# Kernel tuning notes

Measured on AMD Instinct MI355X. Metric: run time of the kernel, lower is better.

Reference implementation:

```python
import jax, jax.numpy as jnp
import numpy as np

HIDDEN = 1024
FFN = 4096
NUM_EXPERTS = 8
TOP_K = 2


def setup_inputs() -> dict:
    key = jax.random.key(0)
    k1, k2, k3, k4, k5 = jax.random.split(key, 5)
    B, T = 4, 2048
    x = jax.random.normal(k1, (B, T, HIDDEN), dtype=jnp.float32)
    # router: nn.Linear(hidden_dim, num_experts)
    bound = 1.0 / np.sqrt(HIDDEN)
    router_w = jax.random.uniform(k2, (NUM_EXPERTS, HIDDEN), dtype=jnp.float32, minval=-bound, maxval=bound)
    router_b = jax.random.uniform(k3, (NUM_EXPERTS,), dtype=jnp.float32, minval=-bound, maxval=bound)
    w1 = jax.random.normal(k4, (NUM_EXPERTS, HIDDEN, FFN), dtype=jnp.float32) * 0.02
    w2 = jax.random.normal(k5, (NUM_EXPERTS, FFN, HIDDEN), dtype=jnp.float32) * 0.02
    return {"x": x, "router_w": router_w, "router_b": router_b, "w1": w1, "w2": w2}


def reference(x, router_w, router_b, w1, w2):
    B, T, H = x.shape
    x_flat = x.reshape(-1, H)                      # [N, H], N = B*T
    logits = x_flat @ router_w.T + router_b        # [N, E]
    probs = jax.nn.softmax(logits, axis=-1)
    topk_w, topk_idx = jax.lax.top_k(probs, TOP_K)  # [N, K]
    topk_w = topk_w / jnp.sum(topk_w, axis=-1, keepdims=True)
    # combine weight per (expert, token): sum_k topk_w[:,k] * onehot(topk_idx[:,k])
    onehot = jax.nn.one_hot(topk_idx, NUM_EXPERTS, dtype=x.dtype)   # [N, K, E]
    combine = jnp.einsum('nk,nke->en', topk_w, onehot)              # [E, N]
    # dense per-expert FFN (math identical to original masked loop: gelu(0)=0)
    hidden = jax.nn.gelu(jnp.einsum('nh,ehf->enf', x_flat, w1), approximate=False)  # [E, N, F]
    expert_out = jnp.einsum('enf,efh->enh', hidden, w2)             # [E, N, H]
    out = jnp.einsum('enh,en->nh', expert_out, combine)             # [N, H]
    return out.reshape(B, T, H)
```

## Files before the change

### kernel.cpp

```cpp
#include <hip/hip_runtime.h>
#include <cstdint>
#include <cstddef>

#define H_DIM 1024
#define F_DIM 4096
#define N_EXP 8
#define N_TOK 8192
#define NK_ASSIGN (N_TOK * 2)
#define MAX_MB 24
#define NMB 32

typedef unsigned short u16;
typedef __attribute__((ext_vector_type(8))) short bf16x8;
typedef __attribute__((ext_vector_type(4))) float f32x4;

__device__ __forceinline__ u16 f2bf(float f) {
  unsigned int u = __float_as_uint(f);
  u += 0x7fffu + ((u >> 16) & 1u);
  return (u16)(u >> 16);
}

__device__ __forceinline__ void load16(const u16* g, u16* l) {
  __builtin_amdgcn_global_load_lds(
      (const __attribute__((address_space(1))) void*)g,
      (__attribute__((address_space(3))) void*)l, 16, 0, 0);
}

__global__ __launch_bounds__(256) void router_kernel(
    const float* __restrict__ x, const float* __restrict__ rw,
    const float* __restrict__ rb, int* __restrict__ topk_idx,
    float* __restrict__ topk_w, u16* __restrict__ xb) {
  const int lane = threadIdx.x & 63;
  const int wid = threadIdx.x >> 6;
  const int t = blockIdx.x * 4 + wid;
  const float4* xr = (const float4*)(x + (size_t)t * H_DIM);
  u16* xo = xb + (size_t)t * H_DIM;
  float acc[N_EXP];
#pragma unroll
  for (int e = 0; e < N_EXP; ++e) acc[e] = 0.f;
#pragma unroll
  for (int j = 0; j < 4; ++j) {
    float4 xv = xr[j * 64 + lane];
    ushort4 u;
    u.x = f2bf(xv.x); u.y = f2bf(xv.y); u.z = f2bf(xv.z); u.w = f2bf(xv.w);
    *(ushort4*)(xo + (size_t)(j * 64 + lane) * 4) = u;
#pragma unroll
    for (int e = 0; e < N_EXP; ++e) {
      float4 wv = ((const float4*)(rw + e * H_DIM))[j * 64 + lane];
      acc[e] += xv.x * wv.x + xv.y * wv.y + xv.z * wv.z + xv.w * wv.w;
    }
  }
#pragma unroll
  for (int off = 32; off > 0; off >>= 1) {
#pragma unroll
    for (int e = 0; e < N_EXP; ++e) acc[e] += __shfl_xor(acc[e], off);
  }
  if (lane == 0) {
    float lg[N_EXP];
#pragma unroll
    for (int e = 0; e < N_EXP; ++e) lg[e] = acc[e] + rb[e];
    int i0 = 0;
    float b0 = lg[0];
#pragma unroll
    for (int e = 1; e < N_EXP; ++e)
      if (lg[e] > b0) { b0 = lg[e]; i0 = e; }
    int i1 = -1;
    float b1 = -3.4e38f;
#pragma unroll
    for (int e = 0; e < N_EXP; ++e)
      if (e != i0 && lg[e] > b1) { b1 = lg[e]; i1 = e; }
    float w0 = 1.f / (1.f + __expf(b1 - b0));
    topk_idx[2 * t] = i0;
    topk_idx[2 * t + 1] = i1;
    topk_w[2 * t] = w0;
    topk_w[2 * t + 1] = 1.f - w0;
  }
}

__global__ __launch_bounds__(256) void hist_kernel(
    const int* __restrict__ topk_idx, int* __restrict__ hist_g) {
  __shared__ int hh[N_EXP];
  const int tid = threadIdx.x;
  if (tid < N_EXP) hh[tid] = 0;
  __syncthreads();
  const int t = blockIdx.x * 256 + tid;
  const int e0 = topk_idx[2 * t], e1 = topk_idx[2 * t + 1];
  atomicAdd(&hh[e0], 1);
  atomicAdd(&hh[e1], 1);
  __syncthreads();
  if (tid < N_EXP) hist_g[blockIdx.x * N_EXP + tid] = hh[tid];
}

__global__ __launch_bounds__(256) void scan_kernel(
    const int* __restrict__ hist_g, int* __restrict__ offsets,
    int* __restrict__ pos_base) {
  __shared__ int sh[NMB * N_EXP];
  __shared__ int pb[NMB * N_EXP];
  const int tid = threadIdx.x;
  sh[tid] = hist_g[tid];
  __syncthreads();
  if (tid == 0) {
    int tot[N_EXP];
    for (int e = 0; e < N_EXP; ++e) tot[e] = 0;
    for (int b = 0; b < NMB; ++b)
      for (int e = 0; e < N_EXP; ++e) tot[e] += sh[b * N_EXP + e];
    int run = 0;
    for (int e = 0; e < N_EXP; ++e) { offsets[e] = run; run += tot[e]; }
    offsets[N_EXP] = run;
    for (int e = 0; e < N_EXP; ++e) {
      int r = offsets[e];
      for (int b = 0; b < NMB; ++b) { pb[b * N_EXP + e] = r; r += sh[b * N_EXP + e]; }
    }
  }
  __syncthreads();
  pos_base[tid] = pb[tid];
}

__global__ __launch_bounds__(256) void scatter_kernel(
    const int* __restrict__ topk_idx, const float* __restrict__ topk_w,
    const int* __restrict__ pos_base, int* __restrict__ assign_token,
    float* __restrict__ assign_gate, int* __restrict__ slot_of) {
  __shared__ int cur[N_EXP];
  __shared__ int pb[N_EXP];
  const int tid = threadIdx.x;
  if (tid < N_EXP) {
    cur[tid] = 0;
    pb[tid] = pos_base[blockIdx.x * N_EXP + tid];
  }
  __syncthreads();
  const int t = blockIdx.x * 256 + tid;
#pragma unroll
  for (int k = 0; k < 2; ++k) {
    int e = topk_idx[2 * t + k];
    int local = atomicAdd(&cur[e], 1);
    int pos = pb[e] + local;
    assign_token[pos] = t;
    assign_gate[pos] = topk_w[2 * t + k];
    slot_of[2 * t + k] = pos;
  }
}

__global__ __launch_bounds__(256) void transpose_cvt(
    const float* __restrict__ in, u16* __restrict__ out, int R, int C) {
  __shared__ u16 lds[64 * 66];
  const int e = blockIdx.z;
  const float* ip = in + (size_t)e * R * C;
  u16* op = out + (size_t)e * R * C;
  const int c0 = blockIdx.x * 64, r0 = blockIdx.y * 64;
  const int tid = threadIdx.x;
  const int tx = tid & 15, ty = tid >> 4;
#pragma unroll
  for (int i = 0; i < 4; ++i) {
    const int r = ty + i * 16;
    float4 v = *(const float4*)(ip + (size_t)(r0 + r) * C + c0 + tx * 4);
    ushort2 u01, u23;
    u01.x = f2bf(v.x); u01.y = f2bf(v.y);
    u23.x = f2bf(v.z); u23.y = f2bf(v.w);
    *(ushort2*)&lds[r * 66 + tx * 4] = u01;
    *(ushort2*)&lds[r * 66 + tx * 4 + 2] = u23;
  }
  __syncthreads();
  const int lane = tid & 63, wid = tid >> 6;
  const int r8 = lane & 7;
#pragma unroll
  for (int s = 0; s < 2; ++s) {
    const int c = s * 32 + wid * 8 + (lane >> 3);
    union { u16 u[8]; uint4 q; } pk;
#pragma unroll
    for (int k = 0; k < 8; ++k) pk.u[k] = lds[(r8 * 8 + k) * 66 + c];
    *(uint4*)(op + (size_t)(c0 + c) * R + r0 + r8 * 8) = pk.q;
  }
}

template <int LDA, int LDB, int LDC, int KITERS, int NXB, bool FIRST>
__global__ __launch_bounds__(256) void moe_gemm(
    const u16* __restrict__ Abase, const u16* __restrict__ Bbase,
    u16* __restrict__ hout, float* __restrict__ yout,
    const int* __restrict__ offsets, const float* __restrict__ assign_gate,
    const int* __restrict__ atok) {
  __shared__ __align__(16) u16 As[128 * 32];
  __shared__ __align__(16) u16 Bs[128 * 32];
  const int flat = blockIdx.x + NXB * (blockIdx.y + MAX_MB * blockIdx.z);
  const int e = flat & 7;
  const int s = flat >> 3;
  const int mb = s % MAX_MB;
  const int n0b = s / MAX_MB;
  const int row0 = offsets[e];
  const int cnt = offsets[e + 1] - row0;
  const int mbase = mb * 128;
  if (mbase >= cnt) return;
  const int mrem = cnt - mbase;
  const int n0 = n0b * 128;
  const int tid = threadIdx.x;
  const int lane = tid & 63;
  const int wid = tid >> 6;
  const int wm = wid & 1, wn = wid >> 1;
  const u16* B = Bbase + (size_t)e * ((size_t)H_DIM * F_DIM);
  const int row16 = lane & 15, quad = lane >> 4;
  const int srow = lane >> 2;
  const int scol = (lane & 3) * 8;

  const u16* Arow[2];
  const u16* Brow[2];
#pragma unroll
  for (int i = 0; i < 2; ++i) {
    const int c = wid * 2 + i;
    const int r = c * 16 + srow;
    const int ra = min(r, mrem - 1);
    if (FIRST) {
      const int tok = atok[row0 + mbase + ra];
      Arow[i] = Abase + (size_t)tok * LDA;
    } else {
      Arow[i] = Abase + (size_t)(row0 + mbase + ra) * LDA;
    }
    Brow[i] = B + (size_t)(n0 + r) * LDB;
  }

  f32x4 acc[4][4];
#pragma unroll
  for (int i = 0; i < 4; ++i)
#pragma unroll
    for (int j = 0; j < 4; ++j)
#pragma unroll
      for (int r = 0; r < 4; ++r) acc[i][j][r] = 0.f;

  for (int kt = 0; kt < KITERS; ++kt) {
    const int k0 = kt * 32;
#pragma unroll
    for (int i = 0; i < 2; ++i) {
      const int c = wid * 2 + i;
      load16(Arow[i] + k0 + scol, &As[c * 512]);
      load16(Brow[i] + k0 + scol, &Bs[c * 512]);
    }
    __syncthreads();
    bf16x8 av[4], bv[4];
#pragma unroll
    for (int mi = 0; mi < 4; ++mi)
      av[mi] = *(const bf16x8*)&As[(wm * 64 + mi * 16 + row16) * 32 + quad * 8];
#pragma unroll
    for (int ni = 0; ni < 4; ++ni)
      bv[ni] = *(const bf16x8*)&Bs[(wn * 64 + ni * 16 + row16) * 32 + quad * 8];
#pragma unroll
    for (int mi = 0; mi < 4; ++mi)
#pragma unroll
      for (int ni = 0; ni < 4; ++ni)
        acc[mi][ni] =
            __builtin_amdgcn_mfma_f32_16x16x32_bf16(av[mi], bv[ni], acc[mi][ni], 0, 0, 0);
    __syncthreads();
  }

  if (FIRST) {
    u16* Cp = hout + (size_t)(row0 + mbase) * LDC + n0;
#pragma unroll
    for (int mi = 0; mi < 4; ++mi) {
#pragma unroll
      for (int r = 0; r < 4; ++r) {
        const int lm = wm * 64 + mi * 16 + quad * 4 + r;
        if (lm < mrem) {
#pragma unroll
          for (int ni = 0; ni < 4; ++ni) {
            float v = acc[mi][ni][r];
            float t = v * (0.7978845608028654f + 0.0356774081363f * v * v);
            v = v / (1.f + __expf(-2.f * t));
            Cp[(size_t)lm * LDC + (wn * 64 + ni * 16 + row16)] = f2bf(v);
          }
        }
      }
    }
  } else {
#pragma unroll
    for (int mi = 0; mi < 4; ++mi) {
#pragma unroll
      for (int r = 0; r < 4; ++r) {
        const int lm = wm * 64 + mi * 16 + quad * 4 + r;
        if (lm < mrem) {
          const int slot = row0 + mbase + lm;
          const float g = assign_gate[slot];
          float* orow = yout + (size_t)slot * LDC + n0;
#pragma unroll
          for (int ni = 0; ni < 4; ++ni)
            orow[wn * 64 + ni * 16 + row16] = acc[mi][ni][r] * g;
        }
      }
    }
  }
}

__global__ __launch_bounds__(256) void combine_kernel(
    const float* __restrict__ ys, const int* __restrict__ slot_of,
    float* __restrict__ out) {
  const int t = blockIdx.x;
  const int s0 = slot_of[2 * t], s1 = slot_of[2 * t + 1];
  const int i = threadIdx.x;
  float4 a = ((const float4*)(ys + (size_t)s0 * H_DIM))[i];
  float4 b = ((const float4*)(ys + (size_t)s1 * H_DIM))[i];
  float4 o;
  o.x = a.x + b.x; o.y = a.y + b.y; o.z = a.z + b.z; o.w = a.w + b.w;
  ((float4*)(out + (size_t)t * H_DIM))[i] = o;
}

extern "C" void kernel_launch(void* const* d_in, const int* in_sizes, int n_in,
                              void* d_out, int out_size, void* d_ws, size_t ws_size,
                              hipStream_t stream) {
  const float* x = (const float*)d_in[0];
  const float* rw = (const float*)d_in[1];
  const float* rb = (const float*)d_in[2];
  const float* w1 = (const float*)d_in[3];
  const float* w2 = (const float*)d_in[4];
  float* out = (float*)d_out;

  char* ws = (char*)d_ws;
  u16* w1b = (u16*)(ws);
  float* y_slot = (float*)(ws);
  u16* w2b = (u16*)(ws + 67108864);
  u16* xb = (u16*)(ws + 134217728);
  u16* h = (u16*)(ws + 167772160);
  int* hist_g = (int*)(ws + 167772160);
  int* pos_base = hist_g + NMB * N_EXP;
  char* meta = ws + 301989888;
  int* offsets = (int*)(meta + 64);
  int* topk_idx = (int*)(meta + 128);
  float* topk_w = (float*)(meta + 128 + 65536);
  int* assign_token = (int*)(meta + 128 + 131072);
  float* assign_gate = (float*)(meta + 128 + 196608);
  int* slot_of = (int*)(meta + 128 + 262144);

  router_kernel<<<N_TOK / 4, 256, 0, stream>>>(x, rw, rb, topk_idx, topk_w, xb);
  hist_kernel<<<NMB, 256, 0, stream>>>(topk_idx, hist_g);
  scan_kernel<<<1, 256, 0, stream>>>(hist_g, offsets, pos_base);
  scatter_kernel<<<NMB, 256, 0, stream>>>(topk_idx, topk_w, pos_base,
                                          assign_token, assign_gate, slot_of);
  transpose_cvt<<<dim3(F_DIM / 64, H_DIM / 64, N_EXP), 256, 0, stream>>>(w1, w1b, H_DIM, F_DIM);
  transpose_cvt<<<dim3(H_DIM / 64, F_DIM / 64, N_EXP), 256, 0, stream>>>(w2, w2b, F_DIM, H_DIM);

  moe_gemm<H_DIM, H_DIM, F_DIM, H_DIM / 32, F_DIM / 128, true>
      <<<dim3(F_DIM / 128, MAX_MB, N_EXP), 256, 0, stream>>>(
          xb, w1b, h, nullptr, offsets, assign_gate, assign_token);
  moe_gemm<F_DIM, F_DIM, H_DIM, F_DIM / 32, H_DIM / 128, false>
      <<<dim3(H_DIM / 128, MAX_MB, N_EXP), 256, 0, stream>>>(
          h, w2b, nullptr, y_slot, offsets, assign_gate, nullptr);
  combine_kernel<<<N_TOK, 256, 0, stream>>>(y_slot, slot_of, out);

  (void)in_sizes; (void)n_in; (void)ws_size;
}
```

Measured before the change: 803.3 us.

## Double GEMM K-tile to 64 with XOR-swizzled LDS and fuse scan into scatter

The MoE GEMM now stages a 64-wide K slice per iteration instead of 32, halving the number of barrier pairs per tile, and uses an XOR swizzle on the LDS column chunks to avoid bank conflicts on the 128-byte rows. Separately, the single-block scan kernel is removed: each scatter block recomputes the prefix totals from the histogram itself, saving one launch. The trade-off is double the LDS footprint per block and redundant scan work in every scatter block.

```diff
diff --git a/kernel.cpp b/kernel.cpp
--- a/kernel.cpp
+++ b/kernel.cpp
@@ -91,13 +91,17 @@
   if (tid < N_EXP) hist_g[blockIdx.x * N_EXP + tid] = hh[tid];
 }
 
-__global__ __launch_bounds__(256) void scan_kernel(
+__global__ __launch_bounds__(256) void scatter_kernel(
+    const int* __restrict__ topk_idx, const float* __restrict__ topk_w,
     const int* __restrict__ hist_g, int* __restrict__ offsets,
-    int* __restrict__ pos_base) {
+    int* __restrict__ assign_token, float* __restrict__ assign_gate,
+    int* __restrict__ slot_of) {
   __shared__ int sh[NMB * N_EXP];
-  __shared__ int pb[NMB * N_EXP];
+  __shared__ int pb[N_EXP];
+  __shared__ int cur[N_EXP];
   const int tid = threadIdx.x;
   sh[tid] = hist_g[tid];
+  if (tid < N_EXP) cur[tid] = 0;
   __syncthreads();
   if (tid == 0) {
     int tot[N_EXP];
@@ -105,27 +109,14 @@
     for (int b = 0; b < NMB; ++b)
       for (int e = 0; e < N_EXP; ++e) tot[e] += sh[b * N_EXP + e];
     int run = 0;
-    for (int e = 0; e < N_EXP; ++e) { offsets[e] = run; run += tot[e]; }
-    offsets[N_EXP] = run;
     for (int e = 0; e < N_EXP; ++e) {
-      int r = offsets[e];
-      for (int b = 0; b < NMB; ++b) { pb[b * N_EXP + e] = r; r += sh[b * N_EXP + e]; }
-    }
-  }
-  __syncthreads();
-  pos_base[tid] = pb[tid];
-}
-
-__global__ __launch_bounds__(256) void scatter_kernel(
-    const int* __restrict__ topk_idx, const float* __restrict__ topk_w,
-    const int* __restrict__ pos_base, int* __restrict__ assign_token,
-    float* __restrict__ assign_gate, int* __restrict__ slot_of) {
-  __shared__ int cur[N_EXP];
-  __shared__ int pb[N_EXP];
-  const int tid = threadIdx.x;
-  if (tid < N_EXP) {
-    cur[tid] = 0;
-    pb[tid] = pos_base[blockIdx.x * N_EXP + tid];
+      if (blockIdx.x == 0) offsets[e] = run;
+      int r = run;
+      for (int b = 0; b < (int)blockIdx.x; ++b) r += sh[b * N_EXP + e];
+      pb[e] = r;
+      run += tot[e];
+    }
+    if (blockIdx.x == 0) offsets[N_EXP] = run;
   }
   __syncthreads();
   const int t = blockIdx.x * 256 + tid;
@@ -178,8 +169,8 @@
     u16* __restrict__ hout, float* __restrict__ yout,
     const int* __restrict__ offsets, const float* __restrict__ assign_gate,
     const int* __restrict__ atok) {
-  __shared__ __align__(16) u16 As[128 * 32];
-  __shared__ __align__(16) u16 Bs[128 * 32];
+  __shared__ __align__(16) u16 As[128 * 64];
+  __shared__ __align__(16) u16 Bs[128 * 64];
   const int flat = blockIdx.x + NXB * (blockIdx.y + MAX_MB * blockIdx.z);
   const int e = flat & 7;
   const int s = flat >> 3;
@@ -197,23 +188,23 @@
   const int wm = wid & 1, wn = wid >> 1;
   const u16* B = Bbase + (size_t)e * ((size_t)H_DIM * F_DIM);
   const int row16 = lane & 15, quad = lane >> 4;
-  const int srow = lane >> 2;
-  const int scol = (lane & 3) * 8;
-
-  const u16* Arow[2];
-  const u16* Brow[2];
-#pragma unroll
-  for (int i = 0; i < 2; ++i) {
-    const int c = wid * 2 + i;
-    const int r = c * 16 + srow;
+  const int sr = lane >> 3;
+  const int scol = ((lane & 7) ^ sr) * 8;
+
+  const u16* Arow[4];
+  const u16* Brow[4];
+#pragma unroll
+  for (int i = 0; i < 4; ++i) {
+    const int c = wid * 4 + i;
+    const int r = c * 8 + sr;
     const int ra = min(r, mrem - 1);
     if (FIRST) {
       const int tok = atok[row0 + mbase + ra];
-      Arow[i] = Abase + (size_t)tok * LDA;
+      Arow[i] = Abase + (size_t)tok * LDA + scol;
     } else {
-      Arow[i] = Abase + (size_t)(row0 + mbase + ra) * LDA;
-    }
-    Brow[i] = B + (size_t)(n0 + r) * LDB;
+      Arow[i] = Abase + (size_t)(row0 + mbase + ra) * LDA + scol;
+    }
+    Brow[i] = B + (size_t)(n0 + r) * LDB + scol;
   }
 
   f32x4 acc[4][4];
@@ -225,27 +216,34 @@
       for (int r = 0; r < 4; ++r) acc[i][j][r] = 0.f;
 
   for (int kt = 0; kt < KITERS; ++kt) {
-    const int k0 = kt * 32;
-#pragma unroll
-    for (int i = 0; i < 2; ++i) {
-      const int c = wid * 2 + i;
-      load16(Arow[i] + k0 + scol, &As[c * 512]);
-      load16(Brow[i] + k0 + scol, &Bs[c * 512]);
+    const int k0 = kt * 64;
+#pragma unroll
+    for (int i = 0; i < 4; ++i) {
+      const int c = wid * 4 + i;
+      load16(Arow[i] + k0, &As[c * 512]);
+      load16(Brow[i] + k0, &Bs[c * 512]);
     }
     __syncthreads();
-    bf16x8 av[4], bv[4];
-#pragma unroll
-    for (int mi = 0; mi < 4; ++mi)
-      av[mi] = *(const bf16x8*)&As[(wm * 64 + mi * 16 + row16) * 32 + quad * 8];
-#pragma unroll
-    for (int ni = 0; ni < 4; ++ni)
-      bv[ni] = *(const bf16x8*)&Bs[(wn * 64 + ni * 16 + row16) * 32 + quad * 8];
-#pragma unroll
-    for (int mi = 0; mi < 4; ++mi)
-#pragma unroll
-      for (int ni = 0; ni < 4; ++ni)
-        acc[mi][ni] =
-            __builtin_amdgcn_mfma_f32_16x16x32_bf16(av[mi], bv[ni], acc[mi][ni], 0, 0, 0);
+#pragma unroll
+    for (int ks = 0; ks < 2; ++ks) {
+      bf16x8 av[4], bv[4];
+#pragma unroll
+      for (int mi = 0; mi < 4; ++mi) {
+        const int r = wm * 64 + mi * 16 + row16;
+        av[mi] = *(const bf16x8*)&As[r * 64 + ((ks * 4 + quad) ^ (r & 7)) * 8];
+      }
+#pragma unroll
+      for (int ni = 0; ni < 4; ++ni) {
+        const int r = wn * 64 + ni * 16 + row16;
+        bv[ni] = *(const bf16x8*)&Bs[r * 64 + ((ks * 4 + quad) ^ (r & 7)) * 8];
+      }
+#pragma unroll
+      for (int mi = 0; mi < 4; ++mi)
+#pragma unroll
+        for (int ni = 0; ni < 4; ++ni)
+          acc[mi][ni] =
+              __builtin_amdgcn_mfma_f32_16x16x32_bf16(av[mi], bv[ni], acc[mi][ni], 0, 0, 0);
+    }
     __syncthreads();
   }
 
@@ -316,7 +314,6 @@
   u16* xb = (u16*)(ws + 134217728);
   u16* h = (u16*)(ws + 167772160);
   int* hist_g = (int*)(ws + 167772160);
-  int* pos_base = hist_g + NMB * N_EXP;
   char* meta = ws + 301989888;
   int* offsets = (int*)(meta + 64);
   int* topk_idx = (int*)(meta + 128);
@@ -327,16 +324,15 @@
 
   router_kernel<<<N_TOK / 4, 256, 0, stream>>>(x, rw, rb, topk_idx, topk_w, xb);
   hist_kernel<<<NMB, 256, 0, stream>>>(topk_idx, hist_g);
-  scan_kernel<<<1, 256, 0, stream>>>(hist_g, offsets, pos_base);
-  scatter_kernel<<<NMB, 256, 0, stream>>>(topk_idx, topk_w, pos_base,
+  scatter_kernel<<<NMB, 256, 0, stream>>>(topk_idx, topk_w, hist_g, offsets,
                                           assign_token, assign_gate, slot_of);
   transpose_cvt<<<dim3(F_DIM / 64, H_DIM / 64, N_EXP), 256, 0, stream>>>(w1, w1b, H_DIM, F_DIM);
   transpose_cvt<<<dim3(H_DIM / 64, F_DIM / 64, N_EXP), 256, 0, stream>>>(w2, w2b, F_DIM, H_DIM);
 
-  moe_gemm<H_DIM, H_DIM, F_DIM, H_DIM / 32, F_DIM / 128, true>
+  moe_gemm<H_DIM, H_DIM, F_DIM, H_DIM / 64, F_DIM / 128, true>
       <<<dim3(F_DIM / 128, MAX_MB, N_EXP), 256, 0, stream>>>(
           xb, w1b, h, nullptr, offsets, assign_gate, assign_token);
-  moe_gemm<F_DIM, F_DIM, H_DIM, F_DIM / 32, H_DIM / 128, false>
+  moe_gemm<F_DIM, F_DIM, H_DIM, F_DIM / 64, H_DIM / 128, false>
       <<<dim3(H_DIM / 128, MAX_MB, N_EXP), 256, 0, stream>>>(
           h, w2b, nullptr, y_slot, offsets, assign_gate, nullptr);
   combine_kernel<<<N_TOK, 256, 0, stream>>>(y_slot, slot_of, out);
```

Result: slower. 907.9 us (+13.0%).
